# Performance work log

Hardware: AMD Instinct MI355X
Metric: run time of the kernel (lower is better)

The kernel has to match this reference:

```python
import jax, jax.numpy as jnp
import numpy as np

PATCH = 16  # patch_size: unfold kernel == stride


def setup_inputs() -> dict:
    key = jax.random.key(0)
    k1, k2 = jax.random.split(key)
    x = jax.random.normal(k1, (32, 128, 128, 128), dtype=jnp.float32)          # [b, n, h, w]
    conv_w = jax.random.normal(k2, (128, 128, 3, 3), dtype=jnp.float32) * 0.02  # [out_c, in_c, kh, kw]
    return {"x": x, "conv_w": conv_w}


def reference(x, conv_w):
    b, n, h, w = x.shape
    p = PATCH
    nh, nw = h // p, w // p
    bn = b * n
    P = nh * nw  # number of patches per (b, n) slice

    # unfold(1, p, p).unfold(2, p, p): [bn, nh, nw, p, p]
    a = x.reshape(bn, nh, p, nw, p).transpose(0, 1, 3, 2, 4).reshape(bn, P, p, p)
    a1 = a.reshape(bn, P, p * p)

    # patch-to-patch affinity + softmax: [bn, P, P]
    f1 = jnp.einsum('bie,bje->bij', a1, a1)
    f_div_C = jax.nn.softmax(f1, axis=-1)

    # AdaptiveAvgPool2d(1) over each patch -> per-patch mean: [bn, P]
    y1 = a.mean(axis=(-2, -1))

    # attention-weighted patch means: [bn, P] -> [b, n, nh, nw]
    y2 = jnp.einsum('bij,bj->bi', f_div_C, y1).reshape(b, n, nh, nw)

    # 3x3 conv, stride 1, SAME padding, no bias
    y2 = jax.lax.conv_general_dilated(
        y2, conv_w, window_strides=(1, 1), padding='SAME',
        dimension_numbers=('NCHW', 'OIHW', 'NCHW'))

    # global average pool -> [b, n, 1, 1]
    return y2.mean(axis=(2, 3), keepdims=True)
```

## Files before the change

kernel.cpp:

```cpp
#include <hip/hip_runtime.h>


#define NP   64
#define PE   256
#define SLICE_ELEMS 16384


__global__ __launch_bounds__(256, 2)
void k1_attn(const float* __restrict__ x, float* __restrict__ y2g) {
    __shared__ __align__(16) float a_lds[NP * PE];
    __shared__ float y1part[4][64];

    const int slice = blockIdx.x;
    const int tid   = threadIdx.x;
    const int wid   = tid >> 6;
    const int lane  = tid & 63;

    const float* xs = x + (size_t)slice * SLICE_ELEMS;

    {
        const float4* xs4 = (const float4*)xs;
        float4 st[16];
#pragma unroll
        for (int it = 0; it < 16; ++it) st[it] = xs4[it * 256 + tid];
#pragma unroll
        for (int it = 0; it < 16; ++it) {
            const int G    = it * 256 + tid;
            const int row  = G >> 5;
            const int col4 = G & 31;
            const int p    = ((row >> 4) << 3) + (col4 >> 2);
            const int m    = ((row & 15) << 2) + (col4 & 3);
            const int sb   = m ^ (p >> 3);
            *(float4*)&a_lds[p * PE + 4 * sb] = st[it];
        }
    }
    __syncthreads();

    {
        const int low = lane & 7, sig = lane >> 3;
        float s = 0.f;
#pragma unroll
        for (int kk = 0; kk < 16; ++kk) {
            const int m  = (wid << 4) + (kk ^ low);
            const int sb = m ^ sig;
            float4 v = *(const float4*)&a_lds[lane * PE + 4 * sb];
            s += (v.x + v.y) + (v.z + v.w);
        }
        y1part[wid][lane] = s;
    }

    const int ti = lane >> 3, tj = lane & 7;
    float acc[8][8];
#pragma unroll
    for (int r = 0; r < 8; ++r)
#pragma unroll
        for (int c = 0; c < 8; ++c) acc[r][c] = 0.f;

#pragma unroll 2
    for (int s = 0; s < 16; ++s) {
        const int m  = (wid << 4) + s;
        const int bi = 4 * (m ^ ti);
        const int bj = 4 * (m ^ tj);
        float4 av[8], bv[8];
#pragma unroll
        for (int r = 0; r < 8; ++r) av[r] = *(const float4*)&a_lds[(8 * ti + r) * PE + bi];
#pragma unroll
        for (int c = 0; c < 8; ++c) bv[c] = *(const float4*)&a_lds[(8 * tj + c) * PE + bj];
#pragma unroll
        for (int r = 0; r < 8; ++r)
#pragma unroll
            for (int c = 0; c < 8; ++c)
                acc[r][c] += av[r].x * bv[c].x + av[r].y * bv[c].y +
                             av[r].z * bv[c].z + av[r].w * bv[c].w;
    }
    __syncthreads();

    float* fp = a_lds;
    if (wid > 0) {
        float* reg = fp + (wid - 1) * (64 * 68) + lane * 68;
#pragma unroll
        for (int r = 0; r < 8; ++r) {
            *(float4*)&reg[r * 8 + 0] = make_float4(acc[r][0], acc[r][1], acc[r][2], acc[r][3]);
            *(float4*)&reg[r * 8 + 4] = make_float4(acc[r][4], acc[r][5], acc[r][6], acc[r][7]);
        }
    }
    __syncthreads();

    if (wid == 0) {
#pragma unroll
        for (int w = 0; w < 3; ++w) {
            const float* reg = fp + w * (64 * 68) + lane * 68;
#pragma unroll
            for (int r = 0; r < 8; ++r) {
                float4 u0 = *(const float4*)&reg[r * 8 + 0];
                float4 u1 = *(const float4*)&reg[r * 8 + 4];
                acc[r][0] += u0.x; acc[r][1] += u0.y; acc[r][2] += u0.z; acc[r][3] += u0.w;
                acc[r][4] += u1.x; acc[r][5] += u1.y; acc[r][6] += u1.z; acc[r][7] += u1.w;
            }
        }

        const float y1v = (y1part[0][lane] + y1part[1][lane] +
                           y1part[2][lane] + y1part[3][lane]) * (1.f / 256.f);
        float y1c[8];
#pragma unroll
        for (int c = 0; c < 8; ++c) y1c[c] = __shfl(y1v, tj * 8 + c);

#pragma unroll
        for (int r = 0; r < 8; ++r) {
            float mx = acc[r][0];
#pragma unroll
            for (int c = 1; c < 8; ++c) mx = fmaxf(mx, acc[r][c]);
            mx = fmaxf(mx, __shfl_xor(mx, 1));
            mx = fmaxf(mx, __shfl_xor(mx, 2));
            mx = fmaxf(mx, __shfl_xor(mx, 4));
            float sum = 0.f, num = 0.f;
#pragma unroll
            for (int c = 0; c < 8; ++c) {
                const float e = __expf(acc[r][c] - mx);
                sum += e;
                num += e * y1c[c];
            }
            sum += __shfl_xor(sum, 1); num += __shfl_xor(num, 1);
            sum += __shfl_xor(sum, 2); num += __shfl_xor(num, 2);
            sum += __shfl_xor(sum, 4); num += __shfl_xor(num, 4);
            if (tj == 0) y2g[(size_t)slice * 64 + 8 * ti + r] = num / sum;
        }
    }
}

__global__ __launch_bounds__(128, 4)
void k2_conv(const float* __restrict__ y2g, const float* __restrict__ cw,
             float* __restrict__ out) {
    __shared__ __align__(16) float Tf[1152];
    const int b = blockIdx.x;
    const int t = threadIdx.x;

    {
        float g[64];
        const float4* s4 = (const float4*)(y2g + ((size_t)b * 128 + t) * 64);
#pragma unroll
        for (int q = 0; q < 16; ++q) {
            float4 v = s4[q];
            g[4 * q + 0] = v.x; g[4 * q + 1] = v.y; g[4 * q + 2] = v.z; g[4 * q + 3] = v.w;
        }
        float R[8], C[8], S = 0.f;
#pragma unroll
        for (int r = 0; r < 8; ++r) { R[r] = 0.f; C[r] = 0.f; }
#pragma unroll
        for (int r = 0; r < 8; ++r)
#pragma unroll
            for (int c = 0; c < 8; ++c) { R[r] += g[8 * r + c]; C[c] += g[8 * r + c]; }
#pragma unroll
        for (int r = 0; r < 8; ++r) S += R[r];
#pragma unroll
        for (int kh = 0; kh < 3; ++kh)
#pragma unroll
            for (int kw = 0; kw < 3; ++kw) {
                float v = S;
                if (kh == 0) v -= R[7]; else if (kh == 2) v -= R[0];
                if (kw == 0) v -= C[7]; else if (kw == 2) v -= C[0];
                if (kh != 1 && kw != 1) {
                    const int er = (kh == 0) ? 7 : 0;
                    const int ec = (kw == 0) ? 7 : 0;
                    v += g[8 * er + ec];
                }
                Tf[t * 9 + kh * 3 + kw] = v;
            }
    }
    __syncthreads();

    {
        float accum = 0.f;
        const float4* wp = (const float4*)(cw + (size_t)t * 1152);
        const float4* Tp = (const float4*)Tf;
#pragma unroll 4
        for (int j = 0; j < 288; ++j) {
            const float4 a  = wp[j];
            const float4 tt = Tp[j];
            accum += a.x * tt.x + a.y * tt.y + a.z * tt.z + a.w * tt.w;
        }
        out[b * 128 + t] = accum * (1.f / 64.f);
    }
}

extern "C" void kernel_launch(void* const* d_in, const int* in_sizes, int n_in,
                              void* d_out, int out_size, void* d_ws, size_t ws_size,
                              hipStream_t stream) {
    const float* x  = (const float*)d_in[0];
    const float* cw = (const float*)d_in[1];
    float* out = (float*)d_out;
    float* y2g = (float*)d_ws;

    hipLaunchKernelGGL(k1_attn, dim3(4096), dim3(256), 0, stream, x, y2g);
    hipLaunchKernelGGL(k2_conv, dim3(32), dim3(128), 0, stream, y2g, cw, out);
}
```

Before: 440.5 us.

## Use bf16 MFMA for patch affinity and coalesce conv weight loads

The attention kernel converts patches to bf16 in LDS and computes the 64x64 Gram matrix with 16x16x32 bf16 MFMA instructions, one row block per wave. This removes the fp32 FMA loop and the cross-wave LDS reduction, and it also computes the patch means during the load. The smaller LDS footprint allows raising occupancy to 4 blocks per CU. The conv kernel stages y2 through LDS and reads weights cooperatively with a 16-lane shuffle reduction to get coalesced loads. bf16 rounding of the logits before softmax risks accuracy drift.

```diff
diff --git a/kernel.cpp b/kernel.cpp
--- a/kernel.cpp
+++ b/kernel.cpp
@@ -1,146 +1,125 @@
 #include <hip/hip_runtime.h>
 
 
-#define NP   64
-#define PE   256
-#define SLICE_ELEMS 16384
+typedef __attribute__((ext_vector_type(8))) short short8;
+typedef __attribute__((ext_vector_type(4))) float f32x4;
 
+#define RS 264
 
-__global__ __launch_bounds__(256, 2)
+__device__ __forceinline__ ushort f2bf(float f) {
+    unsigned u = __float_as_uint(f);
+    u += 0x7FFF + ((u >> 16) & 1);
+    return (ushort)(u >> 16);
+}
+
+__global__ __launch_bounds__(256, 4)
 void k1_attn(const float* __restrict__ x, float* __restrict__ y2g) {
-    __shared__ __align__(16) float a_lds[NP * PE];
-    __shared__ float y1part[4][64];
+    __shared__ __align__(16) ushort A[64 * RS];
+    __shared__ float y1sc[64 * 9];
+    __shared__ float y1f[64];
 
     const int slice = blockIdx.x;
     const int tid   = threadIdx.x;
-    const int wid   = tid >> 6;
     const int lane  = tid & 63;
+    const int w     = tid >> 6;
 
-    const float* xs = x + (size_t)slice * SLICE_ELEMS;
+    const float4* xs4 = (const float4*)(x + (size_t)slice * 16384);
+    float4 st[16];
+#pragma unroll
+    for (int it = 0; it < 16; ++it) st[it] = xs4[it * 256 + tid];
 
-    {
-        const float4* xs4 = (const float4*)xs;
-        float4 st[16];
+    const int pc = (tid & 31) >> 2;
+    const int s  = tid >> 5;
+    const int c4 = tid & 3;
+
 #pragma unroll
-        for (int it = 0; it < 16; ++it) st[it] = xs4[it * 256 + tid];
-#pragma unroll
-        for (int it = 0; it < 16; ++it) {
-            const int G    = it * 256 + tid;
-            const int row  = G >> 5;
-            const int col4 = G & 31;
-            const int p    = ((row >> 4) << 3) + (col4 >> 2);
-            const int m    = ((row & 15) << 2) + (col4 & 3);
-            const int sb   = m ^ (p >> 3);
-            *(float4*)&a_lds[p * PE + 4 * sb] = st[it];
-        }
+    for (int pb = 0; pb < 8; ++pb) {
+        const float4 v0 = st[2 * pb], v1 = st[2 * pb + 1];
+        float part = (v0.x + v0.y + v0.z + v0.w) + (v1.x + v1.y + v1.z + v1.w);
+        part += __shfl_xor(part, 1);
+        part += __shfl_xor(part, 2);
+        if (c4 == 0) y1sc[(tid >> 2) * 9 + pb] = part;
+        const int p = pb * 8 + pc;
+        ushort4 b0 = make_ushort4(f2bf(v0.x), f2bf(v0.y), f2bf(v0.z), f2bf(v0.w));
+        ushort4 b1 = make_ushort4(f2bf(v1.x), f2bf(v1.y), f2bf(v1.z), f2bf(v1.w));
+        *(ushort4*)&A[p * RS + s * 16 + c4 * 4]       = b0;
+        *(ushort4*)&A[p * RS + (8 + s) * 16 + c4 * 4] = b1;
     }
     __syncthreads();
 
-    {
-        const int low = lane & 7, sig = lane >> 3;
-        float s = 0.f;
+    if (tid < 64) {
+        const int opb = tid >> 3, opc = tid & 7;
+        float sum = 0.f;
 #pragma unroll
-        for (int kk = 0; kk < 16; ++kk) {
-            const int m  = (wid << 4) + (kk ^ low);
-            const int sb = m ^ sig;
-            float4 v = *(const float4*)&a_lds[lane * PE + 4 * sb];
-            s += (v.x + v.y) + (v.z + v.w);
-        }
-        y1part[wid][lane] = s;
-    }
-
-    const int ti = lane >> 3, tj = lane & 7;
-    float acc[8][8];
-#pragma unroll
-    for (int r = 0; r < 8; ++r)
-#pragma unroll
-        for (int c = 0; c < 8; ++c) acc[r][c] = 0.f;
-
-#pragma unroll 2
-    for (int s = 0; s < 16; ++s) {
-        const int m  = (wid << 4) + s;
-        const int bi = 4 * (m ^ ti);
-        const int bj = 4 * (m ^ tj);
-        float4 av[8], bv[8];
-#pragma unroll
-        for (int r = 0; r < 8; ++r) av[r] = *(const float4*)&a_lds[(8 * ti + r) * PE + bi];
-#pragma unroll
-        for (int c = 0; c < 8; ++c) bv[c] = *(const float4*)&a_lds[(8 * tj + c) * PE + bj];
-#pragma unroll
-        for (int r = 0; r < 8; ++r)
-#pragma unroll
-            for (int c = 0; c < 8; ++c)
-                acc[r][c] += av[r].x * bv[c].x + av[r].y * bv[c].y +
-                             av[r].z * bv[c].z + av[r].w * bv[c].w;
+        for (int a = 0; a < 8; ++a) sum += y1sc[(a * 8 + opc) * 9 + opb];
+        y1f[tid] = sum * (1.f / 256.f);
     }
     __syncthreads();
 
-    float* fp = a_lds;
-    if (wid > 0) {
-        float* reg = fp + (wid - 1) * (64 * 68) + lane * 68;
+    const int l15 = lane & 15, lg = lane >> 4;
+    const int r0  = w * 16;
+
+    float y1c[4];
 #pragma unroll
-        for (int r = 0; r < 8; ++r) {
-            *(float4*)&reg[r * 8 + 0] = make_float4(acc[r][0], acc[r][1], acc[r][2], acc[r][3]);
-            *(float4*)&reg[r * 8 + 4] = make_float4(acc[r][4], acc[r][5], acc[r][6], acc[r][7]);
+    for (int c = 0; c < 4; ++c) y1c[c] = y1f[c * 16 + l15];
+
+    f32x4 acc[4];
+#pragma unroll
+    for (int c = 0; c < 4; ++c) acc[c] = (f32x4){0.f, 0.f, 0.f, 0.f};
+
+#pragma unroll
+    for (int kk = 0; kk < 8; ++kk) {
+        const int ko = kk * 32 + lg * 8;
+        short8 af = *(const short8*)&A[(r0 + l15) * RS + ko];
+#pragma unroll
+        for (int c = 0; c < 4; ++c) {
+            short8 bf = *(const short8*)&A[(c * 16 + l15) * RS + ko];
+            acc[c] = __builtin_amdgcn_mfma_f32_16x16x32_bf16(af, bf, acc[c], 0, 0, 0);
         }
     }
-    __syncthreads();
-
-    if (wid == 0) {
-#pragma unroll
-        for (int w = 0; w < 3; ++w) {
-            const float* reg = fp + w * (64 * 68) + lane * 68;
-#pragma unroll
-            for (int r = 0; r < 8; ++r) {
-                float4 u0 = *(const float4*)&reg[r * 8 + 0];
-                float4 u1 = *(const float4*)&reg[r * 8 + 4];
-                acc[r][0] += u0.x; acc[r][1] += u0.y; acc[r][2] += u0.z; acc[r][3] += u0.w;
-                acc[r][4] += u1.x; acc[r][5] += u1.y; acc[r][6] += u1.z; acc[r][7] += u1.w;
-            }
-        }
-
-        const float y1v = (y1part[0][lane] + y1part[1][lane] +
-                           y1part[2][lane] + y1part[3][lane]) * (1.f / 256.f);
-        float y1c[8];
-#pragma unroll
-        for (int c = 0; c < 8; ++c) y1c[c] = __shfl(y1v, tj * 8 + c);
 
 #pragma unroll
-        for (int r = 0; r < 8; ++r) {
-            float mx = acc[r][0];
-#pragma unroll
-            for (int c = 1; c < 8; ++c) mx = fmaxf(mx, acc[r][c]);
-            mx = fmaxf(mx, __shfl_xor(mx, 1));
-            mx = fmaxf(mx, __shfl_xor(mx, 2));
-            mx = fmaxf(mx, __shfl_xor(mx, 4));
-            float sum = 0.f, num = 0.f;
-#pragma unroll
-            for (int c = 0; c < 8; ++c) {
-                const float e = __expf(acc[r][c] - mx);
-                sum += e;
-                num += e * y1c[c];
-            }
-            sum += __shfl_xor(sum, 1); num += __shfl_xor(num, 1);
-            sum += __shfl_xor(sum, 2); num += __shfl_xor(num, 2);
-            sum += __shfl_xor(sum, 4); num += __shfl_xor(num, 4);
-            if (tj == 0) y2g[(size_t)slice * 64 + 8 * ti + r] = num / sum;
-        }
+    for (int r = 0; r < 4; ++r) {
+        const float v0 = acc[0][r], v1 = acc[1][r], v2 = acc[2][r], v3 = acc[3][r];
+        float mx = fmaxf(fmaxf(v0, v1), fmaxf(v2, v3));
+        mx = fmaxf(mx, __shfl_xor(mx, 1));
+        mx = fmaxf(mx, __shfl_xor(mx, 2));
+        mx = fmaxf(mx, __shfl_xor(mx, 4));
+        mx = fmaxf(mx, __shfl_xor(mx, 8));
+        const float e0 = __expf(v0 - mx), e1 = __expf(v1 - mx);
+        const float e2 = __expf(v2 - mx), e3 = __expf(v3 - mx);
+        float sum = e0 + e1 + e2 + e3;
+        float num = e0 * y1c[0] + e1 * y1c[1] + e2 * y1c[2] + e3 * y1c[3];
+        sum += __shfl_xor(sum, 1); num += __shfl_xor(num, 1);
+        sum += __shfl_xor(sum, 2); num += __shfl_xor(num, 2);
+        sum += __shfl_xor(sum, 4); num += __shfl_xor(num, 4);
+        sum += __shfl_xor(sum, 8); num += __shfl_xor(num, 8);
+        if (l15 == 0) y2g[(size_t)slice * 64 + r0 + lg * 4 + r] = num / sum;
     }
 }
 
 __global__ __launch_bounds__(128, 4)
 void k2_conv(const float* __restrict__ y2g, const float* __restrict__ cw,
              float* __restrict__ out) {
+    __shared__ __align__(16) float y2s[128 * 68];
     __shared__ __align__(16) float Tf[1152];
     const int b = blockIdx.x;
     const int t = threadIdx.x;
 
+    const float4* src = (const float4*)(y2g + (size_t)b * 8192);
+#pragma unroll
+    for (int it = 0; it < 16; ++it) {
+        const int fi = it * 128 + t;
+        float4 v = src[fi];
+        *(float4*)&y2s[(fi >> 4) * 68 + (fi & 15) * 4] = v;
+    }
+    __syncthreads();
+
     {
         float g[64];
-        const float4* s4 = (const float4*)(y2g + ((size_t)b * 128 + t) * 64);
 #pragma unroll
         for (int q = 0; q < 16; ++q) {
-            float4 v = s4[q];
+            float4 v = *(const float4*)&y2s[t * 68 + q * 4];
             g[4 * q + 0] = v.x; g[4 * q + 1] = v.y; g[4 * q + 2] = v.z; g[4 * q + 3] = v.w;
         }
         float R[8], C[8], S = 0.f;
@@ -170,16 +149,24 @@
     __syncthreads();
 
     {
-        float accum = 0.f;
-        const float4* wp = (const float4*)(cw + (size_t)t * 1152);
-        const float4* Tp = (const float4*)Tf;
-#pragma unroll 4
-        for (int j = 0; j < 288; ++j) {
-            const float4 a  = wp[j];
-            const float4 tt = Tp[j];
-            accum += a.x * tt.x + a.y * tt.y + a.z * tt.z + a.w * tt.w;
+        const int wv = t >> 6, ln = t & 63, gg = ln >> 4, j16 = ln & 15;
+#pragma unroll 2
+        for (int pass = 0; pass < 16; ++pass) {
+            const int oc = pass * 8 + wv * 4 + gg;
+            const float4* wp = (const float4*)(cw + (size_t)oc * 1152);
+            float acc = 0.f;
+#pragma unroll
+            for (int it = 0; it < 18; ++it) {
+                const float4 a  = wp[it * 16 + j16];
+                const float4 tt = *(const float4*)&Tf[(it * 16 + j16) * 4];
+                acc += a.x * tt.x + a.y * tt.y + a.z * tt.z + a.w * tt.w;
+            }
+            acc += __shfl_xor(acc, 1);
+            acc += __shfl_xor(acc, 2);
+            acc += __shfl_xor(acc, 4);
+            acc += __shfl_xor(acc, 8);
+            if (j16 == 0) out[b * 128 + oc] = acc * (1.f / 64.f);
         }
-        out[b * 128 + t] = accum * (1.f / 64.f);
     }
 }
 
```

Result: faster. 375.1 us (-14.8%).
